# Kernel tuning notes

Hardware: AMD Instinct MI355X
Metric: run time of the kernel (lower is better)

The kernel has to match this reference:

```python
import jax, jax.numpy as jnp
import numpy as np

N, E, R, H = 20000, 320000, 8, 4
KG, CC = 128, 4
IN, HID, OUT = 256, 256, 256  # in_channels = KG + 128 (GCN out)
HO1, HO2 = HID // H, OUT // H  # per-head out channels
SLOPE_ACT = 0.01   # nn.LeakyReLU default
SLOPE_ATT = 0.2    # RGATConv negative_slope default


def gcn_conv(x, W, b, src, dst):
    """PyG GCNConv: add self loops, symmetric norm, x@W, scatter-sum, +bias."""
    n = x.shape[0]
    loop = jnp.arange(n, dtype=src.dtype)
    s = jnp.concatenate([src, loop])
    d = jnp.concatenate([dst, loop])
    deg = jnp.zeros((n,), x.dtype).at[d].add(1.0)
    dis = jnp.where(deg > 0, jax.lax.rsqrt(jnp.maximum(deg, 1.0)), 0.0)
    norm = dis[s] * dis[d]                        # [E+N]
    h = x @ W                                     # [n, out]
    out = jax.ops.segment_sum(norm[:, None] * h[s], d, num_segments=n)
    return out + b


def rgat_conv(x, W, q, k, b, src, dst, edge_type, heads, oc):
    """PyG RGATConv (additive-self-attention, across-relation, dim=1, concat)."""
    n = x.shape[0]
    xw = jnp.einsum('ni,rio->rno', x, W)          # [R, n, heads*oc]
    out_i = xw[edge_type, dst]                    # [E, heads*oc]
    out_j = xw[edge_type, src]                    # [E, heads*oc]
    qi = out_i @ q                                # [E, heads]
    kj = out_j @ k                                # [E, heads]
    alpha = jax.nn.leaky_relu(qi + kj, SLOPE_ATT)
    # softmax over incoming edges per destination node (across-relation)
    amax = jax.ops.segment_max(alpha, dst, num_segments=n)[dst]
    ex = jnp.exp(alpha - amax)
    denom = jax.ops.segment_sum(ex, dst, num_segments=n)[dst]
    alpha = ex / denom                            # [E, heads]
    e = src.shape[0]
    msg = (alpha[:, :, None] * out_j.reshape(e, heads, oc)).reshape(e, heads * oc)
    out = jax.ops.segment_sum(msg, dst, num_segments=n) + b
    return out, alpha


def setup_inputs() -> dict:
    key = jax.random.key(0)
    ks = jax.random.split(key, 16)
    d = {}
    d['kg_emb'] = jax.random.normal(ks[0], (N, KG), jnp.float32)
    d['ccle0'] = jax.random.normal(ks[1], (N, CC), jnp.float32)
    d['gcn_w1'] = jax.random.normal(ks[2], (CC, 32), jnp.float32) / np.float32(np.sqrt(CC))
    d['gcn_b1'] = jnp.zeros((32,), jnp.float32)
    d['gcn_w2'] = jax.random.normal(ks[3], (32, 128), jnp.float32) / np.float32(np.sqrt(32))
    d['gcn_b2'] = jnp.zeros((128,), jnp.float32)
    d['rgat1_w'] = jax.random.normal(ks[4], (R, IN, HID), jnp.float32) / np.float32(np.sqrt(IN))
    d['rgat1_q'] = jax.random.normal(ks[5], (HID, H), jnp.float32) / np.float32(np.sqrt(HID))
    d['rgat1_k'] = jax.random.normal(ks[6], (HID, H), jnp.float32) / np.float32(np.sqrt(HID))
    d['rgat1_b'] = jnp.zeros((HID,), jnp.float32)
    d['rgat2_w'] = jax.random.normal(ks[7], (R, HID, OUT), jnp.float32) / np.float32(np.sqrt(HID))
    d['rgat2_q'] = jax.random.normal(ks[8], (OUT, H), jnp.float32) / np.float32(np.sqrt(OUT))
    d['rgat2_k'] = jax.random.normal(ks[9], (OUT, H), jnp.float32) / np.float32(np.sqrt(OUT))
    d['rgat2_b'] = jnp.zeros((OUT,), jnp.float32)
    d['lin_w'] = jax.random.normal(ks[10], (IN, OUT), jnp.float32) / np.float32(np.sqrt(IN))
    d['lin_b'] = jnp.zeros((OUT,), jnp.float32)
    d['edge_index'] = jax.random.randint(ks[11], (2, E), 0, N, jnp.int32)
    d['edge_type'] = jax.random.randint(ks[12], (E,), 0, R, jnp.int32)
    return d


def reference(kg_emb, ccle0, gcn_w1, gcn_b1, gcn_w2, gcn_b2,
              rgat1_w, rgat1_q, rgat1_k, rgat1_b,
              rgat2_w, rgat2_q, rgat2_k, rgat2_b,
              lin_w, lin_b, edge_index, edge_type):
    src, dst = edge_index[0], edge_index[1]
    # ccle_layer: GCN(4->32) -> LeakyReLU -> GCN(32->128)
    c = gcn_conv(ccle0, gcn_w1, gcn_b1, src, dst)
    c = jax.nn.leaky_relu(c, SLOPE_ACT)
    c = gcn_conv(c, gcn_w2, gcn_b2, src, dst)
    # node_id = arange(N): concat(kg_emb, ccle_out)
    x0 = jnp.concatenate([kg_emb, c], axis=1)     # [N, IN]
    h, a1 = rgat_conv(x0, rgat1_w, rgat1_q, rgat1_k, rgat1_b,
                      src, dst, edge_type, H, HO1)
    h = jax.nn.leaky_relu(h, SLOPE_ACT)           # dropout p=0 -> identity
    h, a2 = rgat_conv(h, rgat2_w, rgat2_q, rgat2_k, rgat2_b,
                      src, dst, edge_type, H, HO2)
    out = h + (x0 @ lin_w + lin_b)                # residual through self.lin
    return out, a1, a2
```

## Files before the change

### kernel.cpp

```cpp
#include <hip/hip_runtime.h>
#include <cstdint>

static constexpr int N = 20000;
static constexpr int E = 320000;
static constexpr int R = 8;
static constexpr int H = 4;
static constexpr int C = 256;

using short8 = __attribute__((ext_vector_type(8))) short;
using f32x4  = __attribute__((ext_vector_type(4))) float;
using us4    = __attribute__((ext_vector_type(4))) unsigned short;

__device__ __forceinline__ float lrelu(float x, float s) { return x >= 0.f ? x : s * x; }
__device__ __forceinline__ unsigned short f2bf(float f) {
    unsigned u = __float_as_uint(f);
    unsigned r = (u + 0x7FFFu + ((u >> 16) & 1u)) >> 16;
    return (unsigned short)r;
}
__device__ __forceinline__ float bf2f(unsigned short s) {
    return __uint_as_float(((unsigned)s) << 16);
}

__device__ __forceinline__ void gl2l16(const unsigned short* g, unsigned short* l) {
    __builtin_amdgcn_global_load_lds(
        (const __attribute__((address_space(1))) unsigned int*)g,
        (__attribute__((address_space(3))) unsigned int*)l, 16, 0, 0);
}

__global__ void k_zero_int(int* p, int n) {
    int i = blockIdx.x * blockDim.x + threadIdx.x;
    if (i < n) p[i] = 0;
}

__global__ void k_count(const int* __restrict__ ei, int* __restrict__ cnt) {
    int e = blockIdx.x * blockDim.x + threadIdx.x;
    if (e < E) atomicAdd(&cnt[ei[E + e]], 1);
}

__global__ __launch_bounds__(256) void k_scan_a(const int* __restrict__ cnt,
                                                int* __restrict__ loc,
                                                int* __restrict__ bsum) {
    __shared__ int sm[256];
    int t = threadIdx.x;
    int idx = blockIdx.x * 256 + t;
    int v = (idx < N) ? cnt[idx] : 0;
    sm[t] = v;
    __syncthreads();
#pragma unroll
    for (int off = 1; off < 256; off <<= 1) {
        int u = (t >= off) ? sm[t - off] : 0;
        __syncthreads();
        if (t >= off) sm[t] += u;
        __syncthreads();
    }
    if (idx < N) loc[idx] = sm[t] - v;
    if (t == 255) bsum[blockIdx.x] = sm[255];
}

__global__ __launch_bounds__(256) void k_scan_b(int* __restrict__ bsum, int nb) {
    __shared__ int sm[256];
    int t = threadIdx.x;
    int v = (t < nb) ? bsum[t] : 0;
    sm[t] = v;
    __syncthreads();
#pragma unroll
    for (int off = 1; off < 256; off <<= 1) {
        int u = (t >= off) ? sm[t - off] : 0;
        __syncthreads();
        if (t >= off) sm[t] += u;
        __syncthreads();
    }
    if (t < nb) bsum[t] = sm[t] - v;
}

__global__ __launch_bounds__(256) void k_scan_c(const int* __restrict__ cnt,
                                                const int* __restrict__ loc,
                                                const int* __restrict__ bsum,
                                                int* __restrict__ rowptr,
                                                int* __restrict__ cursor,
                                                float* __restrict__ dis) {
    int idx = blockIdx.x * 256 + threadIdx.x;
    if (idx == 0) rowptr[N] = E;
    if (idx >= N) return;
    int run = bsum[blockIdx.x] + loc[idx];
    rowptr[idx] = run;
    cursor[idx] = run;
    dis[idx] = rsqrtf((float)cnt[idx] + 1.0f);
}

__global__ void k_scatter(const int* __restrict__ ei, const int* __restrict__ et,
                          int* __restrict__ cursor, int* __restrict__ csr_se,
                          int* __restrict__ csr_eid) {
    int e = blockIdx.x * blockDim.x + threadIdx.x;
    if (e >= E) return;
    int d = ei[E + e];
    int pos = atomicAdd(&cursor[d], 1);
    csr_se[pos] = (et[e] << 16) | ei[e];
    csr_eid[pos] = e;
}

__global__ void k_h1(const float* __restrict__ x, const float* __restrict__ W,
                     float* __restrict__ h) {
    int idx = blockIdx.x * blockDim.x + threadIdx.x;
    if (idx >= N * 32) return;
    int n = idx >> 5, f = idx & 31;
    const float* xr = x + n * 4;
    float acc = 0.f;
#pragma unroll
    for (int c = 0; c < 4; ++c) acc += xr[c] * W[c * 32 + f];
    h[idx] = acc;
}

__global__ void k_agg32(const int* __restrict__ rowptr, const int* __restrict__ csr_se,
                        const float* __restrict__ dis, const float* __restrict__ h,
                        const float* __restrict__ b, float* __restrict__ c) {
    int idx = blockIdx.x * blockDim.x + threadIdx.x;
    if (idx >= N * 32) return;
    int d = idx >> 5, f = idx & 31;
    int beg = rowptr[d], end = rowptr[d + 1];
    float acc = 0.f;
    for (int i = beg; i < end; ++i) {
        int s = csr_se[i] & 0xFFFF;
        acc += dis[s] * h[s * 32 + f];
    }
    float dd = dis[d];
    c[idx] = dd * acc + dd * dd * h[idx] + b[f];
}

__global__ void k_h2kg(const float* __restrict__ c1, const float* __restrict__ W,
                       const float* __restrict__ kg, unsigned short* __restrict__ h,
                       float* __restrict__ x0, unsigned short* __restrict__ xb0) {
    int idx = blockIdx.x * blockDim.x + threadIdx.x;
    if (idx >= N * 128) return;
    int n = idx >> 7, f = idx & 127;
    const float* cr = c1 + n * 32;
    float acc = 0.f;
    for (int c = 0; c < 32; ++c) acc += lrelu(cr[c], 0.01f) * W[c * 128 + f];
    h[idx] = f2bf(acc);
    float v = kg[idx];
    x0[n * 256 + f] = v;
    xb0[n * 256 + f] = f2bf(v);
}

__global__ void k_agg128(const int* __restrict__ rowptr, const int* __restrict__ csr_se,
                         const float* __restrict__ dis,
                         const unsigned short* __restrict__ h,
                         const float* __restrict__ b, float* __restrict__ x0,
                         unsigned short* __restrict__ xb0) {
    int idx = blockIdx.x * blockDim.x + threadIdx.x;
    if (idx >= N * 128) return;
    int d = idx >> 7, f = idx & 127;
    int beg = rowptr[d], end = rowptr[d + 1];
    float acc = 0.f;
    int i = beg;
    for (; i + 2 <= end; i += 2) {
        int s0 = csr_se[i] & 0xFFFF;
        int s1 = csr_se[i + 1] & 0xFFFF;
        float d0 = dis[s0], d1 = dis[s1];
        float v0 = bf2f(h[s0 * 128 + f]), v1 = bf2f(h[s1 * 128 + f]);
        acc += d0 * v0 + d1 * v1;
    }
    if (i < end) {
        int s = csr_se[i] & 0xFFFF;
        acc += dis[s] * bf2f(h[s * 128 + f]);
    }
    float dd = dis[d];
    float v = dd * acc + dd * dd * bf2f(h[d * 128 + f]) + b[f];
    x0[d * 256 + 128 + f] = v;
    xb0[d * 256 + 128 + f] = f2bf(v);
}

__global__ __launch_bounds__(256) void k_wqkb(const float* __restrict__ W,
                                              const float* __restrict__ q,
                                              const float* __restrict__ kmat,
                                              unsigned short* __restrict__ wqkb) {
    int w = (blockIdx.x * blockDim.x + threadIdx.x) >> 6;
    int lane = threadIdx.x & 63;
    int r = w >> 8, i = w & 255;
    const float* wr = W + ((size_t)(r * 256 + i)) * 256;
    float4 a = *(const float4*)(wr + lane * 4);
    float aq0 = 0.f, aq1 = 0.f, aq2 = 0.f, aq3 = 0.f;
    float ak0 = 0.f, ak1 = 0.f, ak2 = 0.f, ak3 = 0.f;
    int o = lane * 4;
    const float av[4] = {a.x, a.y, a.z, a.w};
#pragma unroll
    for (int j = 0; j < 4; ++j) {
        float4 qv = *(const float4*)(q + (o + j) * 4);
        float4 kv = *(const float4*)(kmat + (o + j) * 4);
        aq0 += av[j] * qv.x; aq1 += av[j] * qv.y;
        aq2 += av[j] * qv.z; aq3 += av[j] * qv.w;
        ak0 += av[j] * kv.x; ak1 += av[j] * kv.y;
        ak2 += av[j] * kv.z; ak3 += av[j] * kv.w;
    }
#pragma unroll
    for (int d = 1; d < 64; d <<= 1) {
        aq0 += __shfl_xor(aq0, d); aq1 += __shfl_xor(aq1, d);
        aq2 += __shfl_xor(aq2, d); aq3 += __shfl_xor(aq3, d);
        ak0 += __shfl_xor(ak0, d); ak1 += __shfl_xor(ak1, d);
        ak2 += __shfl_xor(ak2, d); ak3 += __shfl_xor(ak3, d);
    }
    if (lane == 0) {
        int nq = r * 4, nk = 32 + r * 4;
        wqkb[(nq + 0) * 256 + i] = f2bf(aq0);
        wqkb[(nq + 1) * 256 + i] = f2bf(aq1);
        wqkb[(nq + 2) * 256 + i] = f2bf(aq2);
        wqkb[(nq + 3) * 256 + i] = f2bf(aq3);
        wqkb[(nk + 0) * 256 + i] = f2bf(ak0);
        wqkb[(nk + 1) * 256 + i] = f2bf(ak1);
        wqkb[(nk + 2) * 256 + i] = f2bf(ak2);
        wqkb[(nk + 3) * 256 + i] = f2bf(ak3);
    }
}

#define QP 264
__global__ __launch_bounds__(256) void k_qnkn_mfma(
    const unsigned short* __restrict__ xb, const unsigned short* __restrict__ wqkb,
    float* __restrict__ qn, float* __restrict__ kn)
{
    __shared__ unsigned short Ws[64 * QP];
    int t = threadIdx.x;
    {
        int r = t >> 2, off = (t & 3) * 64;
#pragma unroll
        for (int i = 0; i < 8; ++i)
            *(uint4*)(&Ws[r * QP + off + i * 8]) =
                *(const uint4*)(wqkb + r * 256 + off + i * 8);
    }
    __syncthreads();
    int wave = t >> 6, lane = t & 63;
    int lrow = lane & 15, kq = lane >> 4;
    int mw = blockIdx.x * 64 + wave * 16;
    int gm = mw + lrow;
    int gmc = gm < N ? gm : N - 1;

    f32x4 acc[4];
#pragma unroll
    for (int j = 0; j < 4; ++j) acc[j] = (f32x4){0.f, 0.f, 0.f, 0.f};

    for (int k0 = 0; k0 < 8; ++k0) {
        short8 af = *(const short8*)(xb + (size_t)gmc * 256 + k0 * 32 + kq * 8);
#pragma unroll
        for (int j = 0; j < 4; ++j) {
            short8 bf4 = *(const short8*)(&Ws[(j * 16 + lrow) * QP + k0 * 32 + kq * 8]);
            acc[j] = __builtin_amdgcn_mfma_f32_16x16x32_bf16(bf4, af, acc[j], 0, 0, 0);
        }
    }
    if (gm < N) {
#pragma unroll
        for (int j = 0; j < 4; ++j) {
            int colb = j * 16 + kq * 4;
            float4 v = {acc[j][0], acc[j][1], acc[j][2], acc[j][3]};
            if (colb < 32) *(float4*)(qn + (size_t)gm * 32 + colb) = v;
            else           *(float4*)(kn + (size_t)gm * 32 + (colb - 32)) = v;
        }
    }
}

__global__ void k_soft(const int* __restrict__ rowptr, const int* __restrict__ csr_se,
                       const int* __restrict__ csr_eid,
                       const float* __restrict__ qn, const float* __restrict__ kn,
                       float* __restrict__ alpha_csr, float* __restrict__ aout) {
    int wid = (blockIdx.x * blockDim.x + threadIdx.x) >> 6;
    int lane = threadIdx.x & 63;
    if (wid >= N) return;
    int d = wid;
    int beg = rowptr[d], end = rowptr[d + 1];
    if (beg >= end) return;
    int slot = lane >> 2, h = lane & 3;
    int nc = (end - beg + 15) >> 4;
    const float* qrow = qn + d * 32;

    auto rawv = [&](int i) {
        int se = csr_se[i];
        int tt = se >> 16, s = se & 0xFFFF;
        return lrelu(qrow[tt * 4 + h] + kn[s * 32 + tt * 4 + h], 0.2f);
    };

    float av[4];
    float m = -1e30f;
    for (int c = 0; c < nc; ++c) {
        int i = beg + c * 16 + slot;
        float v = (i < end) ? rawv(i) : -1e30f;
        if (c < 4) av[c] = v;
        m = fmaxf(m, v);
    }
    m = fmaxf(m, __shfl_xor(m, 4));
    m = fmaxf(m, __shfl_xor(m, 8));
    m = fmaxf(m, __shfl_xor(m, 16));
    m = fmaxf(m, __shfl_xor(m, 32));

    float sum = 0.f;
    for (int c = 0; c < nc; ++c) {
        int i = beg + c * 16 + slot;
        float ex = 0.f;
        if (i < end) {
            float v = (c < 4) ? av[c] : rawv(i);
            ex = expf(v - m);
        }
        if (c < 4) av[c] = ex;
        sum += ex;
    }
    sum += __shfl_xor(sum, 4);
    sum += __shfl_xor(sum, 8);
    sum += __shfl_xor(sum, 16);
    sum += __shfl_xor(sum, 32);
    float inv = 1.f / sum;

    for (int c = 0; c < nc; ++c) {
        int i = beg + c * 16 + slot;
        if (i < end) {
            float ex = (c < 4) ? av[c] : expf(rawv(i) - m);
            float a = ex * inv;
            alpha_csr[i * 4 + h] = a;
            aout[csr_eid[i] * 4 + h] = a;
        }
    }
}

#define WTP 72
__global__ __launch_bounds__(256) void k_wconv_t(const float* __restrict__ W,
                                                 unsigned short* __restrict__ Wt) {
    int bid = blockIdx.x;
    int z = bid >> 4;
    int tile = bid & 15;
    int k0 = (tile >> 2) * 64, n0 = (tile & 3) * 64;
    __shared__ unsigned short T[64 * WTP];
    int t = threadIdx.x;
    const float* Wz = W + ((size_t)z << 16);
    int r = t >> 4;
    int cs = (t & 15) * 4;
#pragma unroll
    for (int rr = 0; rr < 4; ++rr) {
        int k = r + rr * 16;
        float4 v = *(const float4*)(Wz + (size_t)(k0 + k) * 256 + n0 + cs);
        T[(cs + 0) * WTP + k] = f2bf(v.x);
        T[(cs + 1) * WTP + k] = f2bf(v.y);
        T[(cs + 2) * WTP + k] = f2bf(v.z);
        T[(cs + 3) * WTP + k] = f2bf(v.w);
    }
    __syncthreads();
    int n = t >> 2, ck = (t & 3) * 16;
    unsigned short* dst = Wt + ((size_t)z << 16) + (size_t)(n0 + n) * 256 + k0 + ck;
    const unsigned short* srcp = T + n * WTP + ck;
    *(uint4*)(dst) = *(const uint4*)(srcp);
    *(uint4*)(dst + 8) = *(const uint4*)(srcp + 8);
}

#define TM 128
#define TN 128
__global__ __launch_bounds__(256) void gemm_mfma4(
    const unsigned short* __restrict__ A, const unsigned short* __restrict__ Bt,
    unsigned short* __restrict__ Cbf, float* __restrict__ Cf,
    const float* __restrict__ bias, const float* __restrict__ bias2,
    int M, int NZ, int NT, int MT, int zlin)
{
    __shared__ unsigned short As[128 * 32];
    __shared__ unsigned short Bs[128 * 32];

    int bi = blockIdx.x;
    int cx = bi & 7;
    int g = bi >> 3;
    int per = NZ * NT;
    int mh = g / per;
    int j  = g % per;
    int mt = mh * 8 + cx;
    if (mt >= MT) return;
    int z  = j % NZ;
    int nb = j / NZ;
    int m0 = mt * TM;
    int n0 = nb * TN;

    const unsigned short* Bz = Bt + ((size_t)z << 16);
    int t = threadIdx.x;
    int wave = t >> 6, lane = t & 63;
    int wr = wave >> 1, wc = wave & 1;
    int lrow = lane & 15, kq = lane >> 4;

    int sr0 = (wave * 2 + 0) * 16 + (lane >> 2);
    int sr1 = (wave * 2 + 1) * 16 + (lane >> 2);
    int sc = (((lane & 3) ^ ((lane >> 3) & 3))) * 8;
    int gm0 = m0 + sr0; if (gm0 >= M) gm0 = M - 1;
    int gm1 = m0 + sr1; if (gm1 >= M) gm1 = M - 1;
    const unsigned short* gA0 = A + (size_t)gm0 * 256 + sc;
    const unsigned short* gA1 = A + (size_t)gm1 * 256 + sc;
    const unsigned short* gB0 = Bz + (size_t)(n0 + sr0) * 256 + sc;
    const unsigned short* gB1 = Bz + (size_t)(n0 + sr1) * 256 + sc;
    unsigned short* lA0 = &As[(wave * 2 + 0) * 512];
    unsigned short* lA1 = &As[(wave * 2 + 1) * 512];
    unsigned short* lB0 = &Bs[(wave * 2 + 0) * 512];
    unsigned short* lB1 = &Bs[(wave * 2 + 1) * 512];

    int rg = (kq ^ ((lrow >> 1) & 3)) * 8;

    f32x4 acc[4][4];
#pragma unroll
    for (int i = 0; i < 4; ++i)
#pragma unroll
        for (int jj = 0; jj < 4; ++jj) acc[i][jj] = (f32x4){0.f, 0.f, 0.f, 0.f};

    for (int k0 = 0; k0 < 256; k0 += 32) {
        gl2l16(gA0 + k0, lA0);
        gl2l16(gA1 + k0, lA1);
        gl2l16(gB0 + k0, lB0);
        gl2l16(gB1 + k0, lB1);
        __syncthreads();
        short8 af[4], bf4[4];
#pragma unroll
        for (int i = 0; i < 4; ++i)
            af[i] = *(const short8*)(&As[(wr * 64 + i * 16 + lrow) * 32 + rg]);
#pragma unroll
        for (int jj = 0; jj < 4; ++jj)
            bf4[jj] = *(const short8*)(&Bs[(wc * 64 + jj * 16 + lrow) * 32 + rg]);
#pragma unroll
        for (int i = 0; i < 4; ++i)
#pragma unroll
            for (int jj = 0; jj < 4; ++jj)
                acc[i][jj] = __builtin_amdgcn_mfma_f32_16x16x32_bf16(bf4[jj], af[i],
                                                                     acc[i][jj], 0, 0, 0);
        __syncthreads();
    }
    if (z == zlin) {
#pragma unroll
        for (int i = 0; i < 4; ++i) {
            int gm = m0 + wr * 64 + i * 16 + lrow;
            if (gm >= M) continue;
#pragma unroll
            for (int jj = 0; jj < 4; ++jj) {
                int gnb = n0 + wc * 64 + jj * 16 + kq * 4;
                float4 b1 = *(const float4*)(bias + gnb);
                float4 b2 = *(const float4*)(bias2 + gnb);
                float4 v = {acc[i][jj][0] + b1.x + b2.x,
                            acc[i][jj][1] + b1.y + b2.y,
                            acc[i][jj][2] + b1.z + b2.z,
                            acc[i][jj][3] + b1.w + b2.w};
                *(float4*)(Cf + (size_t)gm * 256 + gnb) = v;
            }
        }
    } else {
#pragma unroll
        for (int i = 0; i < 4; ++i) {
            int gm = m0 + wr * 64 + i * 16 + lrow;
            if (gm >= M) continue;
#pragma unroll
            for (int jj = 0; jj < 4; ++jj) {
                int gnb = n0 + wc * 64 + jj * 16 + kq * 4;
                us4 v = {f2bf(acc[i][jj][0]), f2bf(acc[i][jj][1]),
                         f2bf(acc[i][jj][2]), f2bf(acc[i][jj][3])};
                *(us4*)(Cbf + ((size_t)z * M + gm) * 256 + gnb) = v;
            }
        }
    }
}

__global__ __launch_bounds__(256) void k_msg_gather(
    const int* __restrict__ rowptr, const int* __restrict__ csr_se,
    const float* __restrict__ alpha_csr, const unsigned short* __restrict__ xw,
    const float* __restrict__ bias, float* __restrict__ out,
    unsigned short* __restrict__ xbout, int r0, int r1, int first, int act) {
    int node = blockIdx.x * 4 + (threadIdx.x >> 6);
    if (node >= N) return;
    int lane = threadIdx.x & 63;
    int hsel = lane >> 4;
    int beg = rowptr[node], end = rowptr[node + 1];
    float ax = 0.f, ay = 0.f, az = 0.f, aw = 0.f;
    const unsigned short* xwl = xw + lane * 4;

    auto accum = [&](int se, float a) {
        int tt = se >> 16, s = se & 0xFFFF;
        uint2 pv = *(const uint2*)(xwl + ((size_t)tt * N + s) * 256);
        ax += a * __uint_as_float(pv.x << 16);
        ay += a * __uint_as_float(pv.x & 0xFFFF0000u);
        az += a * __uint_as_float(pv.y << 16);
        aw += a * __uint_as_float(pv.y & 0xFFFF0000u);
    };

    if (r0 == 0 && r1 == R) {
        int i = beg;
        for (; i + 4 <= end; i += 4) {
            int se0 = csr_se[i], se1 = csr_se[i + 1];
            int se2 = csr_se[i + 2], se3 = csr_se[i + 3];
            float a0 = alpha_csr[i * 4 + hsel];
            float a1 = alpha_csr[i * 4 + 4 + hsel];
            float a2 = alpha_csr[i * 4 + 8 + hsel];
            float a3 = alpha_csr[i * 4 + 12 + hsel];
            accum(se0, a0); accum(se1, a1); accum(se2, a2); accum(se3, a3);
        }
        for (; i < end; ++i) accum(csr_se[i], alpha_csr[i * 4 + hsel]);
    } else {
        for (int i = beg; i < end; ++i) {
            int se = csr_se[i];
            int tt = se >> 16;
            if (tt >= r0 && tt < r1) {
                int s = se & 0xFFFF;
                float a = alpha_csr[i * 4 + hsel];
                uint2 pv = *(const uint2*)(xwl + ((size_t)(tt - r0) * N + s) * 256);
                ax += a * __uint_as_float(pv.x << 16);
                ay += a * __uint_as_float(pv.x & 0xFFFF0000u);
                az += a * __uint_as_float(pv.y << 16);
                aw += a * __uint_as_float(pv.y & 0xFFFF0000u);
            }
        }
    }

    float* o = out + (size_t)node * 256 + lane * 4;
    float vx, vy, vz, vw;
    if (first) {
        float4 b = *(const float4*)(bias + lane * 4);
        vx = ax + b.x; vy = ay + b.y; vz = az + b.z; vw = aw + b.w;
    } else {
        float4 q = *(const float4*)o;
        vx = q.x + ax; vy = q.y + ay; vz = q.z + az; vw = q.w + aw;
    }
    if (act) {
        vx = lrelu(vx, 0.01f); vy = lrelu(vy, 0.01f);
        vz = lrelu(vz, 0.01f); vw = lrelu(vw, 0.01f);
        us4 xv = {f2bf(vx), f2bf(vy), f2bf(vz), f2bf(vw)};
        *(us4*)(xbout + (size_t)node * 256 + lane * 4) = xv;
    }
    float4 v = {vx, vy, vz, vw};
    *(float4*)o = v;
}

extern "C" void kernel_launch(void* const* d_in, const int* in_sizes, int n_in,
                              void* d_out, int out_size, void* d_ws, size_t ws_size,
                              hipStream_t stream) {
    const float* kg   = (const float*)d_in[0];
    const float* cc0  = (const float*)d_in[1];
    const float* gw1  = (const float*)d_in[2];
    const float* gb1  = (const float*)d_in[3];
    const float* gw2  = (const float*)d_in[4];
    const float* gb2  = (const float*)d_in[5];
    const float* r1w  = (const float*)d_in[6];
    const float* r1q  = (const float*)d_in[7];
    const float* r1k  = (const float*)d_in[8];
    const float* r1b  = (const float*)d_in[9];
    const float* r2w  = (const float*)d_in[10];
    const float* r2q  = (const float*)d_in[11];
    const float* r2k  = (const float*)d_in[12];
    const float* r2b  = (const float*)d_in[13];
    const float* linw = (const float*)d_in[14];
    const float* linb = (const float*)d_in[15];
    const int*   ei   = (const int*)d_in[16];
    const int*   et   = (const int*)d_in[17];

    float* out = (float*)d_out;
    float* a1  = out + (size_t)N * C;
    float* a2  = a1 + (size_t)E * H;

    float* ws = (float*)d_ws;
    size_t off = 0;
    float* dis  = ws + off; off += N;
    float* h1   = ws + off; off += (size_t)N * 32;
    float* c1   = ws + off; off += (size_t)N * 32;
    unsigned short* h2b = (unsigned short*)(ws + off); off += (size_t)N * 64;
    float* x0   = ws + off; off += (size_t)N * C;
    float* hmid = ws + off; off += (size_t)N * C;
    float* qn   = ws + off; off += (size_t)N * R * H;
    float* kn   = ws + off; off += (size_t)N * R * H;
    int* cnt     = (int*)(ws + off); off += N;
    int* rowptr  = (int*)(ws + off); off += N + 1;
    int* cursor  = (int*)(ws + off); off += N;
    int* scanloc = (int*)(ws + off); off += N;
    int* scanbs  = (int*)(ws + off); off += 256;
    int* csr_se  = (int*)(ws + off); off += E;
    int* csr_eid = (int*)(ws + off); off += E;
    float* alpha = ws + off; off += (size_t)E * H;
    unsigned short* xb0 = (unsigned short*)(ws + off); off += (size_t)N * 128;
    unsigned short* xb1 = (unsigned short*)(ws + off); off += (size_t)N * 128;
    unsigned short* wt  = (unsigned short*)(ws + off); off += (size_t)(R + 1) * 32768;
    unsigned short* wtl = wt + ((size_t)R << 16);
    unsigned short* wqkb = (unsigned short*)(ws + off); off += 8192;
    unsigned short* xwb = (unsigned short*)(ws + off);

    size_t fixedB = off * 4;
    int K = R;
    if (ws_size > fixedB) {
        size_t kmax = (ws_size - fixedB) / ((size_t)N * C * 2);
        if (kmax < (size_t)K) K = (int)kmax;
    } else {
        K = 1;
    }
    if (K < 1) K = 1;

    const int B = 256;
    auto cdiv = [](long a, long b) { return (int)((a + b - 1) / b); };
    const int MT = cdiv(N, TM);
    const int NT = C / TN;
    const int NB = cdiv(N, 256);

    k_zero_int<<<cdiv(N, B), B, 0, stream>>>(cnt, N);
    k_count<<<cdiv(E, B), B, 0, stream>>>(ei, cnt);
    k_scan_a<<<NB, 256, 0, stream>>>(cnt, scanloc, scanbs);
    k_scan_b<<<1, 256, 0, stream>>>(scanbs, NB);
    k_scan_c<<<NB, 256, 0, stream>>>(cnt, scanloc, scanbs, rowptr, cursor, dis);
    k_scatter<<<cdiv(E, B), B, 0, stream>>>(ei, et, cursor, csr_se, csr_eid);

    k_h1<<<cdiv((long)N * 32, B), B, 0, stream>>>(cc0, gw1, h1);
    k_agg32<<<cdiv((long)N * 32, B), B, 0, stream>>>(rowptr, csr_se, dis, h1, gb1, c1);
    k_h2kg<<<cdiv((long)N * 128, B), B, 0, stream>>>(c1, gw2, kg, h2b, x0, xb0);
    k_agg128<<<cdiv((long)N * 128, B), B, 0, stream>>>(rowptr, csr_se, dis, h2b,
                                                       gb2, x0, xb0);

    auto rgat = [&](unsigned short* xb, const float* W,
                    const float* q, const float* kk, const float* b,
                    float* obuf, unsigned short* xbout, float* aout,
                    int first, int act, int lin, float* linout,
                    const float* lb1, const float* lb2) {
        k_wqkb<<<512, 256, 0, stream>>>(W, q, kk, wqkb);
        k_qnkn_mfma<<<cdiv(N, 64), B, 0, stream>>>(xb, wqkb, qn, kn);
        k_soft<<<cdiv((long)N * 64, B), B, 0, stream>>>(rowptr, csr_se, csr_eid,
                                                        qn, kn, alpha, aout);
        k_wconv_t<<<R * 16, 256, 0, stream>>>(W, wt);
        for (int r0 = 0; r0 < R; r0 += K) {
            int kc = (R - r0) < K ? (R - r0) : K;
            int addlin = (lin && (r0 + kc == R)) ? 1 : 0;
            int nz = kc + addlin;
            int zl = addlin ? kc : -1;
            int gx = 8 * nz * NT * cdiv(MT, 8);
            gemm_mfma4<<<gx, 256, 0, stream>>>(xb, wt + ((size_t)r0 << 16), xwb,
                                               linout, lb1, lb2,
                                               N, nz, NT, MT, zl);
            int last = (r0 + kc >= R) ? 1 : 0;
            k_msg_gather<<<cdiv(N, 4), 256, 0, stream>>>(
                rowptr, csr_se, alpha, xwb, b, obuf, xbout, r0, r0 + kc,
                (first && r0 == 0) ? 1 : 0, act && last);
        }
    };

    k_wconv_t<<<16, 256, 0, stream>>>(linw, wtl);

    rgat(xb0, r1w, r1q, r1k, r1b, hmid, xb1, a1, 1, 1,
         1, out, linb, r2b);

    rgat(xb1, r2w, r2q, r2k, r2b, out, nullptr, a2, 0, 0,
         0, nullptr, nullptr, nullptr);
}
```

Before: 465.9 us.

## Fuse edge softmax into message gather and fold block-sum scan into final scan

Adds a k_soft_gather kernel that computes the per-destination attention softmax and immediately uses the weights, shared via wave shuffles, to accumulate the gathered bf16 messages. This removes the separate softmax kernel and the alpha_csr round trip through global memory when all relations fit in the workspace. The scan also drops the single-block k_scan_b launch: each k_scan_c block sums the preceding block totals itself. The fused path does extra serial shuffles per edge, and the redundant prefix summation grows with the block index.

```diff
diff --git a/kernel.cpp b/kernel.cpp
--- a/kernel.cpp
+++ b/kernel.cpp
@@ -57,32 +57,28 @@
     if (t == 255) bsum[blockIdx.x] = sm[255];
 }
 
-__global__ __launch_bounds__(256) void k_scan_b(int* __restrict__ bsum, int nb) {
-    __shared__ int sm[256];
-    int t = threadIdx.x;
-    int v = (t < nb) ? bsum[t] : 0;
-    sm[t] = v;
-    __syncthreads();
-#pragma unroll
-    for (int off = 1; off < 256; off <<= 1) {
-        int u = (t >= off) ? sm[t - off] : 0;
-        __syncthreads();
-        if (t >= off) sm[t] += u;
-        __syncthreads();
-    }
-    if (t < nb) bsum[t] = sm[t] - v;
-}
-
 __global__ __launch_bounds__(256) void k_scan_c(const int* __restrict__ cnt,
                                                 const int* __restrict__ loc,
                                                 const int* __restrict__ bsum,
                                                 int* __restrict__ rowptr,
                                                 int* __restrict__ cursor,
                                                 float* __restrict__ dis) {
-    int idx = blockIdx.x * 256 + threadIdx.x;
+    __shared__ int wsum[4];
+    __shared__ int smoff;
+    int t = threadIdx.x;
+    int part = 0;
+    for (int j = t; j < blockIdx.x; j += 256) part += bsum[j];
+#pragma unroll
+    for (int d = 1; d < 64; d <<= 1) part += __shfl_xor(part, d);
+    if ((t & 63) == 0) wsum[t >> 6] = part;
+    __syncthreads();
+    if (t == 0) smoff = wsum[0] + wsum[1] + wsum[2] + wsum[3];
+    __syncthreads();
+    int base = smoff;
+    int idx = blockIdx.x * 256 + t;
     if (idx == 0) rowptr[N] = E;
     if (idx >= N) return;
-    int run = bsum[blockIdx.x] + loc[idx];
+    int run = base + loc[idx];
     rowptr[idx] = run;
     cursor[idx] = run;
     dis[idx] = rsqrtf((float)cnt[idx] + 1.0f);
@@ -317,6 +313,107 @@
     }
 }
 
+__global__ __launch_bounds__(256) void k_soft_gather(
+    const int* __restrict__ rowptr, const int* __restrict__ csr_se,
+    const int* __restrict__ csr_eid,
+    const float* __restrict__ qn, const float* __restrict__ kn,
+    const unsigned short* __restrict__ xw,
+    const float* __restrict__ bias, float* __restrict__ out,
+    unsigned short* __restrict__ xbout, float* __restrict__ aout,
+    int first, int act)
+{
+    int node = blockIdx.x * 4 + (threadIdx.x >> 6);
+    if (node >= N) return;
+    int lane = threadIdx.x & 63;
+    int slot = lane >> 2, h = lane & 3;
+    int hsel = lane >> 4;
+    int beg = rowptr[node], end = rowptr[node + 1];
+    float ax = 0.f, ay = 0.f, az = 0.f, aw = 0.f;
+    const unsigned short* xwl = xw + lane * 4;
+
+    if (beg < end) {
+        int nc = (end - beg + 15) >> 4;
+        const float* qrow = qn + node * 32;
+        auto rawv = [&](int i) {
+            int se = csr_se[i];
+            int tt = se >> 16, s = se & 0xFFFF;
+            return lrelu(qrow[tt * 4 + h] + kn[s * 32 + tt * 4 + h], 0.2f);
+        };
+
+        float av[4];
+        float m = -1e30f;
+        for (int c = 0; c < nc; ++c) {
+            int i = beg + c * 16 + slot;
+            float v = (i < end) ? rawv(i) : -1e30f;
+            if (c < 4) av[c] = v;
+            m = fmaxf(m, v);
+        }
+        m = fmaxf(m, __shfl_xor(m, 4));
+        m = fmaxf(m, __shfl_xor(m, 8));
+        m = fmaxf(m, __shfl_xor(m, 16));
+        m = fmaxf(m, __shfl_xor(m, 32));
+
+        float sum = 0.f;
+        for (int c = 0; c < nc; ++c) {
+            int i = beg + c * 16 + slot;
+            float ex = 0.f;
+            if (i < end) {
+                float v = (c < 4) ? av[c] : rawv(i);
+                ex = expf(v - m);
+            }
+            if (c < 4) av[c] = ex;
+            sum += ex;
+        }
+        sum += __shfl_xor(sum, 4);
+        sum += __shfl_xor(sum, 8);
+        sum += __shfl_xor(sum, 16);
+        sum += __shfl_xor(sum, 32);
+        float inv = 1.f / sum;
+
+        for (int c = 0; c < nc; ++c) {
+            int i = beg + c * 16 + slot;
+            float a = 0.f;
+            int se = 0;
+            if (i < end) {
+                float ex = (c < 4) ? av[c] : expf(rawv(i) - m);
+                a = ex * inv;
+                se = csr_se[i];
+                aout[csr_eid[i] * 4 + h] = a;
+            }
+            int ne = end - (beg + c * 16);
+            if (ne > 16) ne = 16;
+            for (int e = 0; e < ne; ++e) {
+                float ag = __shfl(a, (e << 2) | hsel);
+                int seg  = __shfl(se, e << 2);
+                int tt = seg >> 16, s = seg & 0xFFFF;
+                uint2 pv = *(const uint2*)(xwl + ((size_t)tt * N + s) * 256);
+                ax += ag * __uint_as_float(pv.x << 16);
+                ay += ag * __uint_as_float(pv.x & 0xFFFF0000u);
+                az += ag * __uint_as_float(pv.y << 16);
+                aw += ag * __uint_as_float(pv.y & 0xFFFF0000u);
+            }
+        }
+    }
+
+    float* o = out + (size_t)node * 256 + lane * 4;
+    float vx, vy, vz, vw;
+    if (first) {
+        float4 b = *(const float4*)(bias + lane * 4);
+        vx = ax + b.x; vy = ay + b.y; vz = az + b.z; vw = aw + b.w;
+    } else {
+        float4 q = *(const float4*)o;
+        vx = q.x + ax; vy = q.y + ay; vz = q.z + az; vw = q.w + aw;
+    }
+    if (act) {
+        vx = lrelu(vx, 0.01f); vy = lrelu(vy, 0.01f);
+        vz = lrelu(vz, 0.01f); vw = lrelu(vw, 0.01f);
+        us4 xv = {f2bf(vx), f2bf(vy), f2bf(vz), f2bf(vw)};
+        *(us4*)(xbout + (size_t)node * 256 + lane * 4) = xv;
+    }
+    float4 v = {vx, vy, vz, vw};
+    *(float4*)o = v;
+}
+
 #define WTP 72
 __global__ __launch_bounds__(256) void k_wconv_t(const float* __restrict__ W,
                                                  unsigned short* __restrict__ Wt) {
@@ -465,40 +562,17 @@
     float ax = 0.f, ay = 0.f, az = 0.f, aw = 0.f;
     const unsigned short* xwl = xw + lane * 4;
 
-    auto accum = [&](int se, float a) {
-        int tt = se >> 16, s = se & 0xFFFF;
-        uint2 pv = *(const uint2*)(xwl + ((size_t)tt * N + s) * 256);
-        ax += a * __uint_as_float(pv.x << 16);
-        ay += a * __uint_as_float(pv.x & 0xFFFF0000u);
-        az += a * __uint_as_float(pv.y << 16);
-        aw += a * __uint_as_float(pv.y & 0xFFFF0000u);
-    };
-
-    if (r0 == 0 && r1 == R) {
-        int i = beg;
-        for (; i + 4 <= end; i += 4) {
-            int se0 = csr_se[i], se1 = csr_se[i + 1];
-            int se2 = csr_se[i + 2], se3 = csr_se[i + 3];
-            float a0 = alpha_csr[i * 4 + hsel];
-            float a1 = alpha_csr[i * 4 + 4 + hsel];
-            float a2 = alpha_csr[i * 4 + 8 + hsel];
-            float a3 = alpha_csr[i * 4 + 12 + hsel];
-            accum(se0, a0); accum(se1, a1); accum(se2, a2); accum(se3, a3);
-        }
-        for (; i < end; ++i) accum(csr_se[i], alpha_csr[i * 4 + hsel]);
-    } else {
-        for (int i = beg; i < end; ++i) {
-            int se = csr_se[i];
-            int tt = se >> 16;
-            if (tt >= r0 && tt < r1) {
-                int s = se & 0xFFFF;
-                float a = alpha_csr[i * 4 + hsel];
-                uint2 pv = *(const uint2*)(xwl + ((size_t)(tt - r0) * N + s) * 256);
-                ax += a * __uint_as_float(pv.x << 16);
-                ay += a * __uint_as_float(pv.x & 0xFFFF0000u);
-                az += a * __uint_as_float(pv.y << 16);
-                aw += a * __uint_as_float(pv.y & 0xFFFF0000u);
-            }
+    for (int i = beg; i < end; ++i) {
+        int se = csr_se[i];
+        int tt = se >> 16;
+        if (tt >= r0 && tt < r1) {
+            int s = se & 0xFFFF;
+            float a = alpha_csr[i * 4 + hsel];
+            uint2 pv = *(const uint2*)(xwl + ((size_t)(tt - r0) * N + s) * 256);
+            ax += a * __uint_as_float(pv.x << 16);
+            ay += a * __uint_as_float(pv.x & 0xFFFF0000u);
+            az += a * __uint_as_float(pv.y << 16);
+            aw += a * __uint_as_float(pv.y & 0xFFFF0000u);
         }
     }
 
@@ -591,7 +665,6 @@
     k_zero_int<<<cdiv(N, B), B, 0, stream>>>(cnt, N);
     k_count<<<cdiv(E, B), B, 0, stream>>>(ei, cnt);
     k_scan_a<<<NB, 256, 0, stream>>>(cnt, scanloc, scanbs);
-    k_scan_b<<<1, 256, 0, stream>>>(scanbs, NB);
     k_scan_c<<<NB, 256, 0, stream>>>(cnt, scanloc, scanbs, rowptr, cursor, dis);
     k_scatter<<<cdiv(E, B), B, 0, stream>>>(ei, et, cursor, csr_se, csr_eid);
 
@@ -608,22 +681,33 @@
                     const float* lb1, const float* lb2) {
         k_wqkb<<<512, 256, 0, stream>>>(W, q, kk, wqkb);
         k_qnkn_mfma<<<cdiv(N, 64), B, 0, stream>>>(xb, wqkb, qn, kn);
-        k_soft<<<cdiv((long)N * 64, B), B, 0, stream>>>(rowptr, csr_se, csr_eid,
-                                                        qn, kn, alpha, aout);
         k_wconv_t<<<R * 16, 256, 0, stream>>>(W, wt);
-        for (int r0 = 0; r0 < R; r0 += K) {
-            int kc = (R - r0) < K ? (R - r0) : K;
-            int addlin = (lin && (r0 + kc == R)) ? 1 : 0;
-            int nz = kc + addlin;
-            int zl = addlin ? kc : -1;
+        if (K == R) {
+            int nz = R + (lin ? 1 : 0);
+            int zl = lin ? R : -1;
             int gx = 8 * nz * NT * cdiv(MT, 8);
-            gemm_mfma4<<<gx, 256, 0, stream>>>(xb, wt + ((size_t)r0 << 16), xwb,
-                                               linout, lb1, lb2,
-                                               N, nz, NT, MT, zl);
-            int last = (r0 + kc >= R) ? 1 : 0;
-            k_msg_gather<<<cdiv(N, 4), 256, 0, stream>>>(
-                rowptr, csr_se, alpha, xwb, b, obuf, xbout, r0, r0 + kc,
-                (first && r0 == 0) ? 1 : 0, act && last);
+            gemm_mfma4<<<gx, 512 / 2, 0, stream>>>(xb, wt, xwb, linout, lb1, lb2,
+                                                   N, nz, NT, MT, zl);
+            k_soft_gather<<<cdiv(N, 4), B, 0, stream>>>(
+                rowptr, csr_se, csr_eid, qn, kn, xwb, b, obuf, xbout, aout,
+                first, act);
+        } else {
+            k_soft<<<cdiv((long)N * 64, B), B, 0, stream>>>(rowptr, csr_se, csr_eid,
+                                                            qn, kn, alpha, aout);
+            for (int r0 = 0; r0 < R; r0 += K) {
+                int kc = (R - r0) < K ? (R - r0) : K;
+                int addlin = (lin && (r0 + kc == R)) ? 1 : 0;
+                int nz = kc + addlin;
+                int zl = addlin ? kc : -1;
+                int gx = 8 * nz * NT * cdiv(MT, 8);
+                gemm_mfma4<<<gx, 256, 0, stream>>>(xb, wt + ((size_t)r0 << 16), xwb,
+                                                   linout, lb1, lb2,
+                                                   N, nz, NT, MT, zl);
+                int last = (r0 + kc >= R) ? 1 : 0;
+                k_msg_gather<<<cdiv(N, 4), 256, 0, stream>>>(
+                    rowptr, csr_se, alpha, xwb, b, obuf, xbout, r0, r0 + kc,
+                    (first && r0 == 0) ? 1 : 0, act && last);
+            }
         }
     };
 
```

Result: faster. 455.2 us (-2.3%).
